# Optimization experiments

Measured on AMD Instinct MI355X. Metric: run time of the kernel, lower is better.

Reference implementation:

```python
import jax, jax.numpy as jnp
import numpy as np

N_NODES = 100000
N_EDGES = 1600000
IN_CH = 128
HID = 64


def gcn_conv(x, W, b, src, dst, n):
    """PyG-style GCNConv: add self-loops, symmetric deg^-1/2 normalization."""
    h = x @ W  # [n, out]
    # degree including self-loop, computed from destination (col) indices
    deg = jax.ops.segment_sum(jnp.ones_like(dst, dtype=h.dtype), dst, num_segments=n) + 1.0
    dinv = jax.lax.rsqrt(deg)  # [n]
    norm = dinv[src] * dinv[dst]  # [E]
    agg = jax.ops.segment_sum(h[src] * norm[:, None], dst, num_segments=n)
    agg = agg + h * (1.0 / deg)[:, None]  # self-loop term: norm = 1/deg
    return agg + b


def setup_inputs() -> dict:
    key = jax.random.key(0)
    ks = jax.random.split(key, 6)
    x = jax.random.normal(ks[0], (N_NODES, IN_CH), dtype=jnp.float32)
    edge_index = jax.random.randint(ks[1], (2, N_EDGES), 0, N_NODES, dtype=jnp.int64)
    W1 = jax.random.normal(ks[2], (IN_CH, HID), dtype=jnp.float32) / np.sqrt(IN_CH)
    b1 = jnp.zeros((HID,), dtype=jnp.float32)
    W2 = jax.random.normal(ks[3], (HID, HID), dtype=jnp.float32) / np.sqrt(HID)
    b2 = jnp.zeros((HID,), dtype=jnp.float32)
    Wl = jax.random.normal(ks[4], (HID, 1), dtype=jnp.float32) / np.sqrt(HID)
    bl = jnp.zeros((1,), dtype=jnp.float32)
    return {"x": x, "edge_index": edge_index, "W1": W1, "b1": b1,
            "W2": W2, "b2": b2, "Wl": Wl, "bl": bl}


def reference(x, edge_index, W1, b1, W2, b2, Wl, bl):
    src, dst = edge_index[0], edge_index[1]
    n = x.shape[0]
    h = gcn_conv(x, W1, b1, src, dst, n)
    h = jax.nn.relu(h)
    # dropout: identity in eval mode
    h = gcn_conv(h, W2, b2, src, dst, n)
    h = jax.nn.relu(h)
    out = (h @ Wl + bl)[:, 0]  # [n]
    return out
```

## Files before the change

### kernel.cpp

```cpp
#include <hip/hip_runtime.h>
#include <hip/hip_fp16.h>


#define SHIFT 9
#define BSZ   (1 << SHIFT)
#define NBMAX 256
#define BIN_CH 1024
#define PMAX  11776

using f16x8 = __attribute__((ext_vector_type(8))) _Float16;
using f16x2 = __attribute__((ext_vector_type(2))) _Float16;
using f32x4 = __attribute__((ext_vector_type(4))) float;

__global__ __launch_bounds__(256) void k_bin(const int* __restrict__ src,
                                             const int* __restrict__ dst,
                                             unsigned* __restrict__ binned,
                                             int* __restrict__ gbase,
                                             __half* __restrict__ hs,
                                             int n, int nb, int E) {
    if (blockIdx.x == 0 && threadIdx.x < 8) {
        uint4 z = {0u, 0u, 0u, 0u};
        reinterpret_cast<uint4*>(hs + ((size_t)n << 6))[threadIdx.x] = z;
    }
    __shared__ int h[NBMAX];
    __shared__ int ex[NBMAX + 1];
    __shared__ int cur[NBMAX];
    __shared__ int stmp[256];
    const int t = threadIdx.x;
    const int blk = blockIdx.x;
    const int beg = blk * BIN_CH;
    for (int i = t; i < NBMAX; i += 256) h[i] = 0;
    __syncthreads();
    const int e4 = beg + t * 4;
    const bool act = e4 < E;
    int4 d4 = {0, 0, 0, 0};
    if (act) {
        d4 = *reinterpret_cast<const int4*>(dst + e4);
        atomicAdd(&h[d4.x >> SHIFT], 1);
        atomicAdd(&h[d4.y >> SHIFT], 1);
        atomicAdd(&h[d4.z >> SHIFT], 1);
        atomicAdd(&h[d4.w >> SHIFT], 1);
    }
    __syncthreads();
    const int hv = (t < nb) ? h[t] : 0;
    stmp[t] = hv;
    __syncthreads();
    for (int off = 1; off < 256; off <<= 1) {
        int u = (t >= off) ? stmp[t - off] : 0;
        __syncthreads();
        stmp[t] += u;
        __syncthreads();
    }
    if (t <= nb) ex[t] = stmp[t] - ((t < nb) ? h[t] : 0);
    __syncthreads();
    if (t < nb) cur[t] = ex[t];
    if (t <= nb) gbase[(size_t)blk * (nb + 1) + t] = ex[t];
    __syncthreads();
    if (act) {
        const int4 s4 = *reinterpret_cast<const int4*>(src + e4);
        int b0 = d4.x >> SHIFT, b1 = d4.y >> SHIFT;
        int b2 = d4.z >> SHIFT, b3 = d4.w >> SHIFT;
        int p0 = atomicAdd(&cur[b0], 1);
        int p1 = atomicAdd(&cur[b1], 1);
        int p2 = atomicAdd(&cur[b2], 1);
        int p3 = atomicAdd(&cur[b3], 1);
        binned[beg + p0] = (unsigned)s4.x | ((unsigned)(d4.x & (BSZ - 1)) << 17);
        binned[beg + p1] = (unsigned)s4.y | ((unsigned)(d4.y & (BSZ - 1)) << 17);
        binned[beg + p2] = (unsigned)s4.z | ((unsigned)(d4.z & (BSZ - 1)) << 17);
        binned[beg + p3] = (unsigned)s4.w | ((unsigned)(d4.w & (BSZ - 1)) << 17);
    }
}

#define TD 32
__global__ __launch_bounds__(256) void k_xpose(const int* __restrict__ gbase,
                                               int* __restrict__ gbaseT,
                                               int nblk, int nbp1) {
    __shared__ int tile[TD][TD + 1];
    const int ctiles = (nbp1 + TD - 1) / TD;
    const int bx = blockIdx.x % ctiles;
    const int by = blockIdx.x / ctiles;
    const int c0 = bx * TD, r0 = by * TD;
    const int tx = threadIdx.x & 31, ty = threadIdx.x >> 5;
    for (int dy = ty; dy < TD; dy += 8) {
        int r = r0 + dy, c = c0 + tx;
        tile[dy][tx] = (r < nblk && c < nbp1) ? gbase[(size_t)r * nbp1 + c] : 0;
    }
    __syncthreads();
    for (int dy = ty; dy < TD; dy += 8) {
        int r = c0 + dy, c = r0 + tx;
        if (r < nbp1 && c < nblk)
            gbaseT[(size_t)r * nblk + c] = tile[tx][dy];
    }
}

__global__ __launch_bounds__(1024) void k_bfill(const unsigned* __restrict__ binned,
                                                const int* __restrict__ gbaseT,
                                                int nblk, int nb,
                                                int* __restrict__ rowptr,
                                                int* __restrict__ colidx,
                                                float* __restrict__ dinv, int n) {
    __shared__ unsigned pedges[PMAX];
    __shared__ int segarr[2048];
    __shared__ int stmp[1024];
    __shared__ int cnt[BSZ];
    __shared__ int nbase[BSZ];
    const int b = blockIdx.x;
    const int t = threadIdx.x;
    const int* rowS = gbaseT + (size_t)b * nblk;
    const int* rowE = gbaseT + (size_t)(b + 1) * nblk;
    for (int i = t; i < BSZ; i += 1024) cnt[i] = 0;
    int eb = 0;
    {
        int l0 = 0, l1 = 0;
        if (t < nblk)        { int s0 = rowS[t];        l0 = rowE[t] - s0;        eb += s0; }
        if (t + 1024 < nblk) { int s0 = rowS[t + 1024]; l1 = rowE[t + 1024] - s0; eb += s0; }
        segarr[t] = l0;
        segarr[t + 1024] = l1;
    }
    stmp[t] = eb;
    __syncthreads();
    for (int off = 512; off; off >>= 1) {
        if (t < off) stmp[t] += stmp[t + off];
        __syncthreads();
    }
    const int ebeg = stmp[0];
    __syncthreads();
    const int a0 = segarr[2 * t];
    const int a1 = segarr[2 * t + 1];
    const int ps = a0 + a1;
    stmp[t] = ps;
    __syncthreads();
    for (int off = 1; off < 1024; off <<= 1) {
        int u = (t >= off) ? stmp[t - off] : 0;
        __syncthreads();
        stmp[t] += u;
        __syncthreads();
    }
    const int ecnt = min(stmp[1023], PMAX);
    const int exp2_ = stmp[t] - ps;
    segarr[2 * t] = exp2_;
    segarr[2 * t + 1] = exp2_ + a0;
    __syncthreads();
    for (int blk = t; blk < nblk; blk += 1024) {
        const int s0 = rowS[blk];
        const int c = rowE[blk] - s0;
        const int pos = segarr[blk];
        const unsigned* bp = binned + (size_t)blk * BIN_CH + s0;
        for (int k = 0; k < c; ++k) {
            const int d = pos + k;
            if (d < PMAX) pedges[d] = bp[k];
        }
    }
    __syncthreads();
    for (int j = t; j < ecnt; j += 1024)
        atomicAdd(&cnt[pedges[j] >> 17], 1);
    __syncthreads();
    const int c0 = (t < 256) ? cnt[2 * t] : 0;
    const int c1 = (t < 256) ? cnt[2 * t + 1] : 0;
    const int s2 = c0 + c1;
    stmp[t] = s2;
    __syncthreads();
    for (int off = 1; off < 256; off <<= 1) {
        int u = (t >= off && t < 256) ? stmp[t - off] : 0;
        __syncthreads();
        if (t < 256) stmp[t] += u;
        __syncthreads();
    }
    if (t < 256) {
        const int ex = stmp[t] - s2;
        nbase[2 * t] = ex;
        nbase[2 * t + 1] = ex + c0;
    }
    __syncthreads();
    const int gb9 = b << SHIFT;
    for (int j = t; j < BSZ; j += 1024) {
        const int g = gb9 + j;
        if (g < n) {
            rowptr[g] = (int)(((unsigned)(ebeg + nbase[j]) << 8) |
                              (unsigned)min(cnt[j], 255));
            dinv[g] = rsqrtf((float)cnt[j] + 1.0f);
        }
        cnt[j] = nbase[j];
    }
    __syncthreads();
    for (int j = t; j < ecnt; j += 1024) {
        const unsigned e = pedges[j];
        const int lo = (int)(e >> 17);
        const int off = atomicAdd(&cnt[lo], 1);
        colidx[ebeg + off] = (int)((e & 0x1FFFFu) << 7);
    }
}

template <int K, bool A_FP32>
__global__ __launch_bounds__(256) void k_gemm_mfma(const void* __restrict__ Av,
                                                   const float* __restrict__ W,
                                                   const float* __restrict__ dinv,
                                                   __half* __restrict__ C, int n) {
    constexpr int KP = K + 8;
    __shared__ _Float16 Wt[64 * KP];
    const int tid = threadIdx.x;
    for (int i = tid; i < K * 64; i += 256) {
        int k = i >> 6, c = i & 63;
        Wt[c * KP + k] = (_Float16)W[i];
    }
    __syncthreads();

    const int lane = tid & 63;
    const int wv = tid >> 6;
    const int r16 = lane & 15;
    const int kq = lane >> 4;
    const int rb = blockIdx.x * 64 + wv * 16;
    const int arow = min(rb + r16, n - 1);

    f32x4 acc[4] = {{0.f,0.f,0.f,0.f},{0.f,0.f,0.f,0.f},
                    {0.f,0.f,0.f,0.f},{0.f,0.f,0.f,0.f}};

#pragma unroll
    for (int kk = 0; kk < K; kk += 32) {
        f16x8 a;
        if (A_FP32) {
            const float* Ap = (const float*)Av + (size_t)arow * K + kk + kq * 8;
            float4 f0 = *reinterpret_cast<const float4*>(Ap);
            float4 f1 = *reinterpret_cast<const float4*>(Ap + 4);
            a[0] = (_Float16)f0.x; a[1] = (_Float16)f0.y;
            a[2] = (_Float16)f0.z; a[3] = (_Float16)f0.w;
            a[4] = (_Float16)f1.x; a[5] = (_Float16)f1.y;
            a[6] = (_Float16)f1.z; a[7] = (_Float16)f1.w;
        } else {
            const _Float16* Ap = (const _Float16*)Av + (size_t)arow * K + kk + kq * 8;
            a = *reinterpret_cast<const f16x8*>(Ap);
        }
#pragma unroll
        for (int nt = 0; nt < 4; ++nt) {
            f16x8 b = *reinterpret_cast<const f16x8*>(&Wt[(nt * 16 + r16) * KP + kk + kq * 8]);
            acc[nt] = __builtin_amdgcn_mfma_f32_16x16x32_f16(a, b, acc[nt], 0, 0, 0);
        }
    }

#pragma unroll
    for (int r = 0; r < 4; ++r) {
        const int row = rb + kq * 4 + r;
        if (row < n) {
            const float di = dinv[row];
#pragma unroll
            for (int nt = 0; nt < 4; ++nt)
                C[((size_t)row << 6) + nt * 16 + r16] = __float2half(acc[nt][r] * di);
        }
    }
}

__device__ __forceinline__ void dotu4(float acc[8], uint4 u, f16x2 pl, f16x2 ph) {
    union { uint4 u4; f16x2 h[4]; } v;
    v.u4 = u;
    acc[0] = __builtin_amdgcn_fdot2(v.h[0], pl, acc[0], false);
    acc[1] = __builtin_amdgcn_fdot2(v.h[0], ph, acc[1], false);
    acc[2] = __builtin_amdgcn_fdot2(v.h[1], pl, acc[2], false);
    acc[3] = __builtin_amdgcn_fdot2(v.h[1], ph, acc[3], false);
    acc[4] = __builtin_amdgcn_fdot2(v.h[2], pl, acc[4], false);
    acc[5] = __builtin_amdgcn_fdot2(v.h[2], ph, acc[5], false);
    acc[6] = __builtin_amdgcn_fdot2(v.h[3], pl, acc[6], false);
    acc[7] = __builtin_amdgcn_fdot2(v.h[3], ph, acc[7], false);
}

__device__ __forceinline__ void fold8(float acc[8]) {
#pragma unroll
    for (int m = 8; m <= 32; m <<= 1) {
#pragma unroll
        for (int j = 0; j < 8; ++j)
            acc[j] += __shfl_xor(acc[j], m, 64);
    }
}

__device__ __forceinline__ void tail_node(const char* __restrict__ hsb,
                                          const int* __restrict__ colidx,
                                          unsigned pk, int g, int p,
                                          unsigned dum, float acc[8],
                                          f16x2 pl, f16x2 ph) {
    const int deg = (int)(pk & 255u);
    if (deg <= 32) return;
    const int beg = (int)(pk >> 8);
    const int t = deg - g;
    const unsigned poff = (unsigned)(p << 4);
    const unsigned dumo = dum + poff;
    const int ns = (deg + 7) >> 3;
    for (int k = 4; k < ns; k += 4) {
        const int ik = beg + 8 * k + g;
        unsigned c0 = (unsigned)colidx[ik]      + poff;
        unsigned c1 = (unsigned)colidx[ik + 8]  + poff;
        unsigned c2 = (unsigned)colidx[ik + 16] + poff;
        unsigned c3 = (unsigned)colidx[ik + 24] + poff;
        const int kb = 8 * k;
        uint4 u0 = *reinterpret_cast<const uint4*>(hsb + ((kb      < t) ? c0 : dumo));
        uint4 u1 = *reinterpret_cast<const uint4*>(hsb + ((kb + 8  < t) ? c1 : dumo));
        uint4 u2 = *reinterpret_cast<const uint4*>(hsb + ((kb + 16 < t) ? c2 : dumo));
        uint4 u3 = *reinterpret_cast<const uint4*>(hsb + ((kb + 24 < t) ? c3 : dumo));
        dotu4(acc, u0, pl, ph);
        dotu4(acc, u1, pl, ph);
        dotu4(acc, u2, pl, ph);
        dotu4(acc, u3, pl, ph);
    }
}

__device__ __forceinline__ void gather_quad(const char* __restrict__ hsb,
                                            const int* __restrict__ colidx,
                                            unsigned pk0, unsigned pk1,
                                            unsigned pk2, unsigned pk3,
                                            int g, int p, unsigned dum,
                                            float a0[8], float a1[8],
                                            float a2[8], float a3[8]) {
    const f16x2 pl = {(_Float16)1.0f, (_Float16)0.0f};
    const f16x2 ph = {(_Float16)0.0f, (_Float16)1.0f};
    const int beg0 = (int)(pk0 >> 8), deg0 = (int)(pk0 & 255u);
    const int beg1 = (int)(pk1 >> 8), deg1 = (int)(pk1 & 255u);
    const int beg2 = (int)(pk2 >> 8), deg2 = (int)(pk2 & 255u);
    const int beg3 = (int)(pk3 >> 8), deg3 = (int)(pk3 & 255u);
    const int t0 = deg0 - g, t1 = deg1 - g, t2 = deg2 - g, t3 = deg3 - g;
    const unsigned poff = (unsigned)(p << 4);
    const unsigned dumo = dum + poff;
    const int ia = beg0 + g, ib = beg1 + g, ic = beg2 + g, id = beg3 + g;
    unsigned a_0 = (unsigned)colidx[ia]      + poff;
    unsigned a_1 = (unsigned)colidx[ia + 8]  + poff;
    unsigned a_2 = (unsigned)colidx[ia + 16] + poff;
    unsigned a_3 = (unsigned)colidx[ia + 24] + poff;
    unsigned b_0 = (unsigned)colidx[ib]      + poff;
    unsigned b_1 = (unsigned)colidx[ib + 8]  + poff;
    unsigned b_2 = (unsigned)colidx[ib + 16] + poff;
    unsigned b_3 = (unsigned)colidx[ib + 24] + poff;
    unsigned c_0 = (unsigned)colidx[ic]      + poff;
    unsigned c_1 = (unsigned)colidx[ic + 8]  + poff;
    unsigned c_2 = (unsigned)colidx[ic + 16] + poff;
    unsigned c_3 = (unsigned)colidx[ic + 24] + poff;
    unsigned d_0 = (unsigned)colidx[id]      + poff;
    unsigned d_1 = (unsigned)colidx[id + 8]  + poff;
    unsigned d_2 = (unsigned)colidx[id + 16] + poff;
    unsigned d_3 = (unsigned)colidx[id + 24] + poff;
    unsigned oa0 = (0  < t0) ? a_0 : dumo;
    unsigned oa1 = (8  < t0) ? a_1 : dumo;
    unsigned oa2 = (16 < t0) ? a_2 : dumo;
    unsigned oa3 = (24 < t0) ? a_3 : dumo;
    unsigned ob0 = (0  < t1) ? b_0 : dumo;
    unsigned ob1 = (8  < t1) ? b_1 : dumo;
    unsigned ob2 = (16 < t1) ? b_2 : dumo;
    unsigned ob3 = (24 < t1) ? b_3 : dumo;
    unsigned oc0 = (0  < t2) ? c_0 : dumo;
    unsigned oc1 = (8  < t2) ? c_1 : dumo;
    unsigned oc2 = (16 < t2) ? c_2 : dumo;
    unsigned oc3 = (24 < t2) ? c_3 : dumo;
    unsigned od0 = (0  < t3) ? d_0 : dumo;
    unsigned od1 = (8  < t3) ? d_1 : dumo;
    unsigned od2 = (16 < t3) ? d_2 : dumo;
    unsigned od3 = (24 < t3) ? d_3 : dumo;
    uint4 ua0 = *reinterpret_cast<const uint4*>(hsb + oa0);
    uint4 ua1 = *reinterpret_cast<const uint4*>(hsb + oa1);
    uint4 ua2 = *reinterpret_cast<const uint4*>(hsb + oa2);
    uint4 ua3 = *reinterpret_cast<const uint4*>(hsb + oa3);
    uint4 ub0 = *reinterpret_cast<const uint4*>(hsb + ob0);
    uint4 ub1 = *reinterpret_cast<const uint4*>(hsb + ob1);
    uint4 ub2 = *reinterpret_cast<const uint4*>(hsb + ob2);
    uint4 ub3 = *reinterpret_cast<const uint4*>(hsb + ob3);
    uint4 uc0 = *reinterpret_cast<const uint4*>(hsb + oc0);
    uint4 uc1 = *reinterpret_cast<const uint4*>(hsb + oc1);
    uint4 uc2 = *reinterpret_cast<const uint4*>(hsb + oc2);
    uint4 uc3 = *reinterpret_cast<const uint4*>(hsb + oc3);
    uint4 ud0 = *reinterpret_cast<const uint4*>(hsb + od0);
    uint4 ud1 = *reinterpret_cast<const uint4*>(hsb + od1);
    uint4 ud2 = *reinterpret_cast<const uint4*>(hsb + od2);
    uint4 ud3 = *reinterpret_cast<const uint4*>(hsb + od3);
    dotu4(a0, ua0, pl, ph);
    dotu4(a0, ua1, pl, ph);
    dotu4(a0, ua2, pl, ph);
    dotu4(a0, ua3, pl, ph);
    dotu4(a1, ub0, pl, ph);
    dotu4(a1, ub1, pl, ph);
    dotu4(a1, ub2, pl, ph);
    dotu4(a1, ub3, pl, ph);
    dotu4(a2, uc0, pl, ph);
    dotu4(a2, uc1, pl, ph);
    dotu4(a2, uc2, pl, ph);
    dotu4(a2, uc3, pl, ph);
    dotu4(a3, ud0, pl, ph);
    dotu4(a3, ud1, pl, ph);
    dotu4(a3, ud2, pl, ph);
    dotu4(a3, ud3, pl, ph);
    tail_node(hsb, colidx, pk0, g, p, dum, a0, pl, ph);
    tail_node(hsb, colidx, pk1, g, p, dum, a1, pl, ph);
    tail_node(hsb, colidx, pk2, g, p, dum, a2, pl, ph);
    tail_node(hsb, colidx, pk3, g, p, dum, a3, pl, ph);
    fold8(a0);
    fold8(a1);
    fold8(a2);
    fold8(a3);
}

__device__ __forceinline__ void sel4(float a[8], int nsel, const float a0[8],
                                     const float a1[8], const float a2[8],
                                     const float a3[8]) {
#pragma unroll
    for (int j = 0; j < 8; ++j) {
        float x01 = (nsel & 1) ? a1[j] : a0[j];
        float x23 = (nsel & 1) ? a3[j] : a2[j];
        a[j] = (nsel & 2) ? x23 : x01;
    }
}

__global__ __launch_bounds__(256) void k_agg_relu(const __half* __restrict__ hs,
                                                  const int* __restrict__ rowptr,
                                                  const int* __restrict__ colidx,
                                                  const float* __restrict__ dinv,
                                                  const float* __restrict__ b,
                                                  __half* __restrict__ out, int n) {
    const int wv = threadIdx.x >> 6;
    const int i0 = blockIdx.x * 16 + wv * 4;
    const int lane = threadIdx.x & 63;
    if (i0 >= n) return;
    const int g = lane >> 3, p = lane & 7;
    const int ic1 = min(i0 + 1, n - 1);
    const int ic2 = min(i0 + 2, n - 1);
    const int ic3 = min(i0 + 3, n - 1);
    const int nsel = g & 3;
    const int it = i0 + nsel;
    const int iw = min(it, n - 1);
    const unsigned pk0 = (unsigned)rowptr[i0];
    const unsigned pk1 = (unsigned)rowptr[ic1];
    const unsigned pk2 = (unsigned)rowptr[ic2];
    const unsigned pk3 = (unsigned)rowptr[ic3];
    uint4 su = *reinterpret_cast<const uint4*>(hs + ((size_t)iw << 6) + (p << 3));
    const float di = dinv[iw];
    float a0[8] = {}, a1[8] = {}, a2[8] = {}, a3[8] = {};
    gather_quad((const char*)hs, colidx, pk0, pk1, pk2, pk3, g, p,
                (unsigned)n << 7, a0, a1, a2, a3);
    if (lane < 32 && it < n) {
        const f16x2 pl = {(_Float16)1.0f, (_Float16)0.0f};
        const f16x2 ph = {(_Float16)0.0f, (_Float16)1.0f};
        float a[8];
        sel4(a, nsel, a0, a1, a2, a3);
        dotu4(a, su, pl, ph);
        float4 b0 = *reinterpret_cast<const float4*>(b + (p << 3));
        float4 b1 = *reinterpret_cast<const float4*>(b + (p << 3) + 4);
        __half2 h0 = __halves2half2(__float2half(fmaxf(fmaf(a[0], di, b0.x), 0.f)),
                                    __float2half(fmaxf(fmaf(a[1], di, b0.y), 0.f)));
        __half2 h1 = __halves2half2(__float2half(fmaxf(fmaf(a[2], di, b0.z), 0.f)),
                                    __float2half(fmaxf(fmaf(a[3], di, b0.w), 0.f)));
        __half2 h2 = __halves2half2(__float2half(fmaxf(fmaf(a[4], di, b1.x), 0.f)),
                                    __float2half(fmaxf(fmaf(a[5], di, b1.y), 0.f)));
        __half2 h3 = __halves2half2(__float2half(fmaxf(fmaf(a[6], di, b1.z), 0.f)),
                                    __float2half(fmaxf(fmaf(a[7], di, b1.w), 0.f)));
        uint4 u;
        u.x = *reinterpret_cast<unsigned*>(&h0);
        u.y = *reinterpret_cast<unsigned*>(&h1);
        u.z = *reinterpret_cast<unsigned*>(&h2);
        u.w = *reinterpret_cast<unsigned*>(&h3);
        *reinterpret_cast<uint4*>(out + ((size_t)it << 6) + (p << 3)) = u;
    }
}

__global__ __launch_bounds__(256) void k_agg_head(const __half* __restrict__ hs,
                                                  const int* __restrict__ rowptr,
                                                  const int* __restrict__ colidx,
                                                  const float* __restrict__ dinv,
                                                  const float* __restrict__ b2,
                                                  const float* __restrict__ Wl,
                                                  const float* __restrict__ bl,
                                                  float* __restrict__ out, int n) {
    const int wv = threadIdx.x >> 6;
    const int i0 = blockIdx.x * 16 + wv * 4;
    const int lane = threadIdx.x & 63;
    if (i0 >= n) return;
    const int g = lane >> 3, p = lane & 7;
    const int ic1 = min(i0 + 1, n - 1);
    const int ic2 = min(i0 + 2, n - 1);
    const int ic3 = min(i0 + 3, n - 1);
    const int nsel = g & 3;
    const int it = i0 + nsel;
    const int iw = min(it, n - 1);
    const unsigned pk0 = (unsigned)rowptr[i0];
    const unsigned pk1 = (unsigned)rowptr[ic1];
    const unsigned pk2 = (unsigned)rowptr[ic2];
    const unsigned pk3 = (unsigned)rowptr[ic3];
    uint4 su = *reinterpret_cast<const uint4*>(hs + ((size_t)iw << 6) + (p << 3));
    const float di = dinv[iw];
    float a0[8] = {}, a1[8] = {}, a2[8] = {}, a3[8] = {};
    gather_quad((const char*)hs, colidx, pk0, pk1, pk2, pk3, g, p,
                (unsigned)n << 7, a0, a1, a2, a3);
    const f16x2 pl = {(_Float16)1.0f, (_Float16)0.0f};
    const f16x2 ph = {(_Float16)0.0f, (_Float16)1.0f};
    float a[8];
    sel4(a, nsel, a0, a1, a2, a3);
    dotu4(a, su, pl, ph);
    float4 b0 = *reinterpret_cast<const float4*>(b2 + (p << 3));
    float4 b1 = *reinterpret_cast<const float4*>(b2 + (p << 3) + 4);
    float4 w0 = *reinterpret_cast<const float4*>(Wl + (p << 3));
    float4 w1 = *reinterpret_cast<const float4*>(Wl + (p << 3) + 4);
    float v = fmaxf(fmaf(a[0], di, b0.x), 0.f) * w0.x
            + fmaxf(fmaf(a[1], di, b0.y), 0.f) * w0.y
            + fmaxf(fmaf(a[2], di, b0.z), 0.f) * w0.z
            + fmaxf(fmaf(a[3], di, b0.w), 0.f) * w0.w
            + fmaxf(fmaf(a[4], di, b1.x), 0.f) * w1.x
            + fmaxf(fmaf(a[5], di, b1.y), 0.f) * w1.y
            + fmaxf(fmaf(a[6], di, b1.z), 0.f) * w1.z
            + fmaxf(fmaf(a[7], di, b1.w), 0.f) * w1.w;
    v += __shfl_xor(v, 1, 64);
    v += __shfl_xor(v, 2, 64);
    v += __shfl_xor(v, 4, 64);
    if (p == 0 && g < 4 && it < n) out[it] = v + bl[0];
}

extern "C" void kernel_launch(void* const* d_in, const int* in_sizes, int n_in,
                              void* d_out, int out_size, void* d_ws, size_t ws_size,
                              hipStream_t stream) {
    const float* x  = (const float*)d_in[0];
    const int*   ei = (const int*)d_in[1];
    const float* W1 = (const float*)d_in[2];
    const float* b1 = (const float*)d_in[3];
    const float* W2 = (const float*)d_in[4];
    const float* b2 = (const float*)d_in[5];
    const float* Wl = (const float*)d_in[6];
    const float* bl = (const float*)d_in[7];
    float* out = (float*)d_out;

    const int n = in_sizes[0] / 128;
    const int E = in_sizes[1] / 2;
    const int* src = ei;
    const int* dst = ei + E;
    const int nb = (n + BSZ - 1) >> SHIFT;
    const int nblk = (E + BIN_CH - 1) / BIN_CH;

    char* ws = (char*)d_ws;
    size_t o = 0;
    auto alloc = [&](size_t bytes) {
        void* p = ws + o;
        o = (o + bytes + 255) & ~(size_t)255;
        return p;
    };
    float* dinv    = (float*)alloc((size_t)n * 4);
    int*   rowptr  = (int*)  alloc((size_t)(n + 1) * 4);
    int*   colidx  = (int*)  alloc(((size_t)E + 64) * 4);
    int*   gbase   = (int*)  alloc((size_t)nblk * (nb + 1) * 4);
    int*   gbaseT  = (int*)  alloc((size_t)(nb + 1) * nblk * 4);
    __half* hs     = (__half*)alloc((size_t)(n + 1) * 64 * 2);
    __half* bufA   = (__half*)alloc((size_t)n * 64 * 2);
    unsigned* binned = (unsigned*)alloc(((size_t)nblk * BIN_CH) * 4);

    k_bin<<<nblk, 256, 0, stream>>>(src, dst, binned, gbase, hs, n, nb, E);
    const int ctiles = (nb + 1 + TD - 1) / TD;
    const int rtiles = (nblk + TD - 1) / TD;
    k_xpose<<<ctiles * rtiles, 256, 0, stream>>>(gbase, gbaseT, nblk, nb + 1);
    k_bfill<<<nb, 1024, 0, stream>>>(binned, gbaseT, nblk, nb, rowptr, colidx,
                                     dinv, n);

    k_gemm_mfma<128, true><<<(n + 63) / 64, 256, 0, stream>>>(x, W1, dinv, hs, n);
    k_agg_relu<<<(n + 15) / 16, 256, 0, stream>>>(hs, rowptr, colidx, dinv, b1,
                                                  bufA, n);

    k_gemm_mfma<64, false><<<(n + 63) / 64, 256, 0, stream>>>(bufA, W2, dinv, hs, n);
    k_agg_head<<<(n + 15) / 16, 256, 0, stream>>>(hs, rowptr, colidx, dinv, b2,
                                                  Wl, bl, out, n);
}
```

Baseline: 134.3 us.

## Replace CSR colidx with fixed 32-slot padded neighbor table plus overflow

Each node's neighbor list is now stored in a fixed 32-slot row (cfix), with padding slots pre-filled with the dummy-row offset. Edges beyond 32 go to a per-bucket overflow array sized OCAP. This drops the global edge-base reduction in bfill and the per-slot degree masking in the gather loop, and makes index loads aligned and predictable. In exchange, bfill writes n*32 ints including padding, which is more memory traffic than E ints. Overflow per bucket is capped at OCAP, which risks dropping edges for buckets with many high-degree nodes.

```diff
diff --git a/kernel.cpp b/kernel.cpp
--- a/kernel.cpp
+++ b/kernel.cpp
@@ -7,6 +7,7 @@
 #define NBMAX 256
 #define BIN_CH 1024
 #define PMAX  11776
+#define OCAP  1024
 
 using f16x8 = __attribute__((ext_vector_type(8))) _Float16;
 using f16x2 = __attribute__((ext_vector_type(2))) _Float16;
@@ -97,33 +98,26 @@
                                                 const int* __restrict__ gbaseT,
                                                 int nblk, int nb,
                                                 int* __restrict__ rowptr,
-                                                int* __restrict__ colidx,
+                                                int* __restrict__ cfix,
+                                                int* __restrict__ ovf,
                                                 float* __restrict__ dinv, int n) {
     __shared__ unsigned pedges[PMAX];
     __shared__ int segarr[2048];
     __shared__ int stmp[1024];
     __shared__ int cnt[BSZ];
-    __shared__ int nbase[BSZ];
+    __shared__ int obase[BSZ];
     const int b = blockIdx.x;
     const int t = threadIdx.x;
     const int* rowS = gbaseT + (size_t)b * nblk;
     const int* rowE = gbaseT + (size_t)(b + 1) * nblk;
     for (int i = t; i < BSZ; i += 1024) cnt[i] = 0;
-    int eb = 0;
     {
         int l0 = 0, l1 = 0;
-        if (t < nblk)        { int s0 = rowS[t];        l0 = rowE[t] - s0;        eb += s0; }
-        if (t + 1024 < nblk) { int s0 = rowS[t + 1024]; l1 = rowE[t + 1024] - s0; eb += s0; }
+        if (t < nblk)        l0 = rowE[t] - rowS[t];
+        if (t + 1024 < nblk) l1 = rowE[t + 1024] - rowS[t + 1024];
         segarr[t] = l0;
         segarr[t + 1024] = l1;
     }
-    stmp[t] = eb;
-    __syncthreads();
-    for (int off = 512; off; off >>= 1) {
-        if (t < off) stmp[t] += stmp[t + off];
-        __syncthreads();
-    }
-    const int ebeg = stmp[0];
     __syncthreads();
     const int a0 = segarr[2 * t];
     const int a1 = segarr[2 * t + 1];
@@ -155,9 +149,9 @@
     for (int j = t; j < ecnt; j += 1024)
         atomicAdd(&cnt[pedges[j] >> 17], 1);
     __syncthreads();
-    const int c0 = (t < 256) ? cnt[2 * t] : 0;
-    const int c1 = (t < 256) ? cnt[2 * t + 1] : 0;
-    const int s2 = c0 + c1;
+    const int v0 = (t < 256) ? max(cnt[2 * t] - 32, 0) : 0;
+    const int v1 = (t < 256) ? max(cnt[2 * t + 1] - 32, 0) : 0;
+    const int s2 = v0 + v1;
     stmp[t] = s2;
     __syncthreads();
     for (int off = 1; off < 256; off <<= 1) {
@@ -168,26 +162,36 @@
     }
     if (t < 256) {
         const int ex = stmp[t] - s2;
-        nbase[2 * t] = ex;
-        nbase[2 * t + 1] = ex + c0;
+        obase[2 * t] = ex;
+        obase[2 * t + 1] = ex + v0;
     }
     __syncthreads();
     const int gb9 = b << SHIFT;
+    const int dum = (int)((unsigned)n << 7);
     for (int j = t; j < BSZ; j += 1024) {
         const int g = gb9 + j;
         if (g < n) {
-            rowptr[g] = (int)(((unsigned)(ebeg + nbase[j]) << 8) |
-                              (unsigned)min(cnt[j], 255));
-            dinv[g] = rsqrtf((float)cnt[j] + 1.0f);
+            const int dg = cnt[j];
+            rowptr[g] = (int)(((unsigned)(b * OCAP + obase[j]) << 8) |
+                              (unsigned)min(dg, 255));
+            dinv[g] = rsqrtf((float)dg + 1.0f);
         }
-        cnt[j] = nbase[j];
-    }
+    }
+    for (int sx = t; sx < BSZ * 32; sx += 1024) {
+        const int j = sx >> 5, slot = sx & 31;
+        const int g = gb9 + j;
+        if (g < n && slot >= cnt[j]) cfix[(size_t)g * 32 + slot] = dum;
+    }
+    __syncthreads();
+    for (int i = t; i < BSZ; i += 1024) cnt[i] = 0;
     __syncthreads();
     for (int j = t; j < ecnt; j += 1024) {
         const unsigned e = pedges[j];
         const int lo = (int)(e >> 17);
         const int off = atomicAdd(&cnt[lo], 1);
-        colidx[ebeg + off] = (int)((e & 0x1FFFFu) << 7);
+        const int so = (int)((e & 0x1FFFFu) << 7);
+        if (off < 32) cfix[(size_t)(gb9 + lo) * 32 + off] = so;
+        else          ovf[b * OCAP + obase[lo] + off - 32] = so;
     }
 }
 
@@ -272,23 +276,23 @@
 }
 
 __device__ __forceinline__ void tail_node(const char* __restrict__ hsb,
-                                          const int* __restrict__ colidx,
+                                          const int* __restrict__ ovf,
                                           unsigned pk, int g, int p,
                                           unsigned dum, float acc[8],
                                           f16x2 pl, f16x2 ph) {
     const int deg = (int)(pk & 255u);
     if (deg <= 32) return;
-    const int beg = (int)(pk >> 8);
+    const int obeg = (int)(pk >> 8);
     const int t = deg - g;
     const unsigned poff = (unsigned)(p << 4);
     const unsigned dumo = dum + poff;
     const int ns = (deg + 7) >> 3;
     for (int k = 4; k < ns; k += 4) {
-        const int ik = beg + 8 * k + g;
-        unsigned c0 = (unsigned)colidx[ik]      + poff;
-        unsigned c1 = (unsigned)colidx[ik + 8]  + poff;
-        unsigned c2 = (unsigned)colidx[ik + 16] + poff;
-        unsigned c3 = (unsigned)colidx[ik + 24] + poff;
+        const int ik = obeg + 8 * (k - 4) + g;
+        unsigned c0 = (unsigned)ovf[ik]      + poff;
+        unsigned c1 = (unsigned)ovf[ik + 8]  + poff;
+        unsigned c2 = (unsigned)ovf[ik + 16] + poff;
+        unsigned c3 = (unsigned)ovf[ik + 24] + poff;
         const int kb = 8 * k;
         uint4 u0 = *reinterpret_cast<const uint4*>(hsb + ((kb      < t) ? c0 : dumo));
         uint4 u1 = *reinterpret_cast<const uint4*>(hsb + ((kb + 8  < t) ? c1 : dumo));
@@ -302,7 +306,9 @@
 }
 
 __device__ __forceinline__ void gather_quad(const char* __restrict__ hsb,
-                                            const int* __restrict__ colidx,
+                                            const int* __restrict__ cfix,
+                                            const int* __restrict__ ovf,
+                                            int ic0, int ic1, int ic2, int ic3,
                                             unsigned pk0, unsigned pk1,
                                             unsigned pk2, unsigned pk3,
                                             int g, int p, unsigned dum,
@@ -310,46 +316,27 @@
                                             float a2[8], float a3[8]) {
     const f16x2 pl = {(_Float16)1.0f, (_Float16)0.0f};
     const f16x2 ph = {(_Float16)0.0f, (_Float16)1.0f};
-    const int beg0 = (int)(pk0 >> 8), deg0 = (int)(pk0 & 255u);
-    const int beg1 = (int)(pk1 >> 8), deg1 = (int)(pk1 & 255u);
-    const int beg2 = (int)(pk2 >> 8), deg2 = (int)(pk2 & 255u);
-    const int beg3 = (int)(pk3 >> 8), deg3 = (int)(pk3 & 255u);
-    const int t0 = deg0 - g, t1 = deg1 - g, t2 = deg2 - g, t3 = deg3 - g;
     const unsigned poff = (unsigned)(p << 4);
-    const unsigned dumo = dum + poff;
-    const int ia = beg0 + g, ib = beg1 + g, ic = beg2 + g, id = beg3 + g;
-    unsigned a_0 = (unsigned)colidx[ia]      + poff;
-    unsigned a_1 = (unsigned)colidx[ia + 8]  + poff;
-    unsigned a_2 = (unsigned)colidx[ia + 16] + poff;
-    unsigned a_3 = (unsigned)colidx[ia + 24] + poff;
-    unsigned b_0 = (unsigned)colidx[ib]      + poff;
-    unsigned b_1 = (unsigned)colidx[ib + 8]  + poff;
-    unsigned b_2 = (unsigned)colidx[ib + 16] + poff;
-    unsigned b_3 = (unsigned)colidx[ib + 24] + poff;
-    unsigned c_0 = (unsigned)colidx[ic]      + poff;
-    unsigned c_1 = (unsigned)colidx[ic + 8]  + poff;
-    unsigned c_2 = (unsigned)colidx[ic + 16] + poff;
-    unsigned c_3 = (unsigned)colidx[ic + 24] + poff;
-    unsigned d_0 = (unsigned)colidx[id]      + poff;
-    unsigned d_1 = (unsigned)colidx[id + 8]  + poff;
-    unsigned d_2 = (unsigned)colidx[id + 16] + poff;
-    unsigned d_3 = (unsigned)colidx[id + 24] + poff;
-    unsigned oa0 = (0  < t0) ? a_0 : dumo;
-    unsigned oa1 = (8  < t0) ? a_1 : dumo;
-    unsigned oa2 = (16 < t0) ? a_2 : dumo;
-    unsigned oa3 = (24 < t0) ? a_3 : dumo;
-    unsigned ob0 = (0  < t1) ? b_0 : dumo;
-    unsigned ob1 = (8  < t1) ? b_1 : dumo;
-    unsigned ob2 = (16 < t1) ? b_2 : dumo;
-    unsigned ob3 = (24 < t1) ? b_3 : dumo;
-    unsigned oc0 = (0  < t2) ? c_0 : dumo;
-    unsigned oc1 = (8  < t2) ? c_1 : dumo;
-    unsigned oc2 = (16 < t2) ? c_2 : dumo;
-    unsigned oc3 = (24 < t2) ? c_3 : dumo;
-    unsigned od0 = (0  < t3) ? d_0 : dumo;
-    unsigned od1 = (8  < t3) ? d_1 : dumo;
-    unsigned od2 = (16 < t3) ? d_2 : dumo;
-    unsigned od3 = (24 < t3) ? d_3 : dumo;
+    const int b0 = ic0 * 32 + g;
+    const int b1 = ic1 * 32 + g;
+    const int b2 = ic2 * 32 + g;
+    const int b3 = ic3 * 32 + g;
+    unsigned oa0 = (unsigned)cfix[b0]      + poff;
+    unsigned oa1 = (unsigned)cfix[b0 + 8]  + poff;
+    unsigned oa2 = (unsigned)cfix[b0 + 16] + poff;
+    unsigned oa3 = (unsigned)cfix[b0 + 24] + poff;
+    unsigned ob0 = (unsigned)cfix[b1]      + poff;
+    unsigned ob1 = (unsigned)cfix[b1 + 8]  + poff;
+    unsigned ob2 = (unsigned)cfix[b1 + 16] + poff;
+    unsigned ob3 = (unsigned)cfix[b1 + 24] + poff;
+    unsigned oc0 = (unsigned)cfix[b2]      + poff;
+    unsigned oc1 = (unsigned)cfix[b2 + 8]  + poff;
+    unsigned oc2 = (unsigned)cfix[b2 + 16] + poff;
+    unsigned oc3 = (unsigned)cfix[b2 + 24] + poff;
+    unsigned od0 = (unsigned)cfix[b3]      + poff;
+    unsigned od1 = (unsigned)cfix[b3 + 8]  + poff;
+    unsigned od2 = (unsigned)cfix[b3 + 16] + poff;
+    unsigned od3 = (unsigned)cfix[b3 + 24] + poff;
     uint4 ua0 = *reinterpret_cast<const uint4*>(hsb + oa0);
     uint4 ua1 = *reinterpret_cast<const uint4*>(hsb + oa1);
     uint4 ua2 = *reinterpret_cast<const uint4*>(hsb + oa2);
@@ -382,10 +369,10 @@
     dotu4(a3, ud1, pl, ph);
     dotu4(a3, ud2, pl, ph);
     dotu4(a3, ud3, pl, ph);
-    tail_node(hsb, colidx, pk0, g, p, dum, a0, pl, ph);
-    tail_node(hsb, colidx, pk1, g, p, dum, a1, pl, ph);
-    tail_node(hsb, colidx, pk2, g, p, dum, a2, pl, ph);
-    tail_node(hsb, colidx, pk3, g, p, dum, a3, pl, ph);
+    tail_node(hsb, ovf, pk0, g, p, dum, a0, pl, ph);
+    tail_node(hsb, ovf, pk1, g, p, dum, a1, pl, ph);
+    tail_node(hsb, ovf, pk2, g, p, dum, a2, pl, ph);
+    tail_node(hsb, ovf, pk3, g, p, dum, a3, pl, ph);
     fold8(a0);
     fold8(a1);
     fold8(a2);
@@ -405,7 +392,8 @@
 
 __global__ __launch_bounds__(256) void k_agg_relu(const __half* __restrict__ hs,
                                                   const int* __restrict__ rowptr,
-                                                  const int* __restrict__ colidx,
+                                                  const int* __restrict__ cfix,
+                                                  const int* __restrict__ ovf,
                                                   const float* __restrict__ dinv,
                                                   const float* __restrict__ b,
                                                   __half* __restrict__ out, int n) {
@@ -414,21 +402,22 @@
     const int lane = threadIdx.x & 63;
     if (i0 >= n) return;
     const int g = lane >> 3, p = lane & 7;
+    const int ic0 = i0;
     const int ic1 = min(i0 + 1, n - 1);
     const int ic2 = min(i0 + 2, n - 1);
     const int ic3 = min(i0 + 3, n - 1);
     const int nsel = g & 3;
     const int it = i0 + nsel;
     const int iw = min(it, n - 1);
-    const unsigned pk0 = (unsigned)rowptr[i0];
+    const unsigned pk0 = (unsigned)rowptr[ic0];
     const unsigned pk1 = (unsigned)rowptr[ic1];
     const unsigned pk2 = (unsigned)rowptr[ic2];
     const unsigned pk3 = (unsigned)rowptr[ic3];
     uint4 su = *reinterpret_cast<const uint4*>(hs + ((size_t)iw << 6) + (p << 3));
     const float di = dinv[iw];
     float a0[8] = {}, a1[8] = {}, a2[8] = {}, a3[8] = {};
-    gather_quad((const char*)hs, colidx, pk0, pk1, pk2, pk3, g, p,
-                (unsigned)n << 7, a0, a1, a2, a3);
+    gather_quad((const char*)hs, cfix, ovf, ic0, ic1, ic2, ic3,
+                pk0, pk1, pk2, pk3, g, p, (unsigned)n << 7, a0, a1, a2, a3);
     if (lane < 32 && it < n) {
         const f16x2 pl = {(_Float16)1.0f, (_Float16)0.0f};
         const f16x2 ph = {(_Float16)0.0f, (_Float16)1.0f};
@@ -456,7 +445,8 @@
 
 __global__ __launch_bounds__(256) void k_agg_head(const __half* __restrict__ hs,
                                                   const int* __restrict__ rowptr,
-                                                  const int* __restrict__ colidx,
+                                                  const int* __restrict__ cfix,
+                                                  const int* __restrict__ ovf,
                                                   const float* __restrict__ dinv,
                                                   const float* __restrict__ b2,
                                                   const float* __restrict__ Wl,
@@ -467,21 +457,22 @@
     const int lane = threadIdx.x & 63;
     if (i0 >= n) return;
     const int g = lane >> 3, p = lane & 7;
+    const int ic0 = i0;
     const int ic1 = min(i0 + 1, n - 1);
     const int ic2 = min(i0 + 2, n - 1);
     const int ic3 = min(i0 + 3, n - 1);
     const int nsel = g & 3;
     const int it = i0 + nsel;
     const int iw = min(it, n - 1);
-    const unsigned pk0 = (unsigned)rowptr[i0];
+    const unsigned pk0 = (unsigned)rowptr[ic0];
     const unsigned pk1 = (unsigned)rowptr[ic1];
     const unsigned pk2 = (unsigned)rowptr[ic2];
     const unsigned pk3 = (unsigned)rowptr[ic3];
     uint4 su = *reinterpret_cast<const uint4*>(hs + ((size_t)iw << 6) + (p << 3));
     const float di = dinv[iw];
     float a0[8] = {}, a1[8] = {}, a2[8] = {}, a3[8] = {};
-    gather_quad((const char*)hs, colidx, pk0, pk1, pk2, pk3, g, p,
-                (unsigned)n << 7, a0, a1, a2, a3);
+    gather_quad((const char*)hs, cfix, ovf, ic0, ic1, ic2, ic3,
+                pk0, pk1, pk2, pk3, g, p, (unsigned)n << 7, a0, a1, a2, a3);
     const f16x2 pl = {(_Float16)1.0f, (_Float16)0.0f};
     const f16x2 ph = {(_Float16)0.0f, (_Float16)1.0f};
     float a[8];
@@ -534,7 +525,8 @@
     };
     float* dinv    = (float*)alloc((size_t)n * 4);
     int*   rowptr  = (int*)  alloc((size_t)(n + 1) * 4);
-    int*   colidx  = (int*)  alloc(((size_t)E + 64) * 4);
+    int*   cfix    = (int*)  alloc((size_t)n * 32 * 4);
+    int*   ovf     = (int*)  alloc(((size_t)nb * OCAP + 64) * 4);
     int*   gbase   = (int*)  alloc((size_t)nblk * (nb + 1) * 4);
     int*   gbaseT  = (int*)  alloc((size_t)(nb + 1) * nblk * 4);
     __half* hs     = (__half*)alloc((size_t)(n + 1) * 64 * 2);
@@ -545,14 +537,14 @@
     const int ctiles = (nb + 1 + TD - 1) / TD;
     const int rtiles = (nblk + TD - 1) / TD;
     k_xpose<<<ctiles * rtiles, 256, 0, stream>>>(gbase, gbaseT, nblk, nb + 1);
-    k_bfill<<<nb, 1024, 0, stream>>>(binned, gbaseT, nblk, nb, rowptr, colidx,
-                                     dinv, n);
+    k_bfill<<<nb, 1024, 0, stream>>>(binned, gbaseT, nblk, nb, rowptr, cfix,
+                                     ovf, dinv, n);
 
     k_gemm_mfma<128, true><<<(n + 63) / 64, 256, 0, stream>>>(x, W1, dinv, hs, n);
-    k_agg_relu<<<(n + 15) / 16, 256, 0, stream>>>(hs, rowptr, colidx, dinv, b1,
-                                                  bufA, n);
+    k_agg_relu<<<(n + 15) / 16, 256, 0, stream>>>(hs, rowptr, cfix, ovf, dinv,
+                                                  b1, bufA, n);
 
     k_gemm_mfma<64, false><<<(n + 63) / 64, 256, 0, stream>>>(bufA, W2, dinv, hs, n);
-    k_agg_head<<<(n + 15) / 16, 256, 0, stream>>>(hs, rowptr, colidx, dinv, b2,
-                                                  Wl, bl, out, n);
-}
+    k_agg_head<<<(n + 15) / 16, 256, 0, stream>>>(hs, rowptr, cfix, ovf, dinv,
+                                                  b2, Wl, bl, out, n);
+}
```

Result: no change. 135.8 us (+1.1%).
